# Kernel optimization log

Hardware: AMD Instinct MI355X
Metric: run time of the kernel (lower is better)

The kernel has to match this reference:

```python
import jax, jax.numpy as jnp
import numpy as np

K = 16  # centroids per codebook (4-bit LUT indices, blink-mm convention)


def _im2col(x, kh, kw, stride, pad):
    # x: [B, C, H, W] -> [B, P, C*kh*kw] with channel-major feature ordering
    # (each length-(kh*kw) subvector is one channel's patch, matching the
    #  per-channel codebook layout of the 3x3 AMM conv).
    B, C, H, W = x.shape
    xp = jnp.pad(x, ((0, 0), (0, 0), (pad, pad), (pad, pad)))
    Ho = (H + 2 * pad - kh) // stride + 1
    Wo = (W + 2 * pad - kw) // stride + 1
    cols = [xp[:, :, i:i + stride * Ho:stride, j:j + stride * Wo:stride]
            for i in range(kh) for j in range(kw)]  # fixed small loop (<=9)
    feat = jnp.stack(cols, axis=2)                      # [B, C, kh*kw, Ho, Wo]
    feat = feat.reshape(B, C * kh * kw, Ho, Wo)
    feat = feat.transpose(0, 2, 3, 1).reshape(B, Ho * Wo, C * kh * kw)
    return feat, Ho, Wo


def _amm_conv_bn_act(x, centroids, lut, scale, bias, kernel, stride, pad, relu):
    # Product-quantization approximate matmul conv:
    #  1) im2col, split feature dim D into ncodebooks subspaces of dim dsub
    #  2) nearest-centroid (L2) assignment per subspace -> 4-bit index
    #  3) gather+accumulate precomputed LUT dot products over codebooks
    #  4) folded BatchNorm affine + optional ReLU
    feat, Ho, Wo = _im2col(x, kernel, kernel, stride, pad)
    B, P, D = feat.shape
    ncb, k, dsub = centroids.shape
    xs = feat.reshape(B, P, ncb, dsub)
    dots = jnp.einsum('bpcd,ckd->bpck', xs, centroids)          # [B,P,ncb,K]
    c2 = jnp.sum(centroids * centroids, axis=-1)                # [ncb,K]
    idx = jnp.argmin(c2[None, None] - 2.0 * dots, axis=-1)      # [B,P,ncb]
    onehot = jax.nn.one_hot(idx, k, dtype=x.dtype)              # [B,P,ncb,K]
    out = jnp.einsum('bpck,cko->bpo', onehot, lut)              # LUT accumulate
    out = out * scale + bias                                    # folded BN
    if relu:
        out = jax.nn.relu(out)
    Cout = lut.shape[-1]
    return out.reshape(B, Ho, Wo, Cout).transpose(0, 3, 1, 2)


def setup_inputs() -> dict:
    key = jax.random.key(0)
    ks = jax.random.split(key, 16)
    inplanes, planes, width = 1024, 256, 256
    B, H, W = 32, 14, 14
    d = {}
    d['x'] = jax.random.normal(ks[0], (B, inplanes, H, W), dtype=jnp.float32)
    d['c1_centroids'] = jax.random.normal(ks[1], (inplanes // 4, K, 4), dtype=jnp.float32)
    d['c1_lut'] = jax.random.normal(ks[2], (inplanes // 4, K, width), dtype=jnp.float32) * 0.1
    d['c1_scale'] = jax.random.uniform(ks[3], (width,), dtype=jnp.float32, minval=0.5, maxval=1.5)
    d['c1_bias'] = jax.random.normal(ks[4], (width,), dtype=jnp.float32) * 0.1
    d['c2_centroids'] = jax.random.normal(ks[5], (width, K, 9), dtype=jnp.float32)
    d['c2_lut'] = jax.random.normal(ks[6], (width, K, width), dtype=jnp.float32) * 0.1
    d['c2_scale'] = jax.random.uniform(ks[7], (width,), dtype=jnp.float32, minval=0.5, maxval=1.5)
    d['c2_bias'] = jax.random.normal(ks[8], (width,), dtype=jnp.float32) * 0.1
    d['c3_centroids'] = jax.random.normal(ks[9], (width // 4, K, 4), dtype=jnp.float32)
    d['c3_lut'] = jax.random.normal(ks[10], (width // 4, K, planes * 4), dtype=jnp.float32) * 0.1
    d['c3_scale'] = jax.random.uniform(ks[11], (planes * 4,), dtype=jnp.float32, minval=0.5, maxval=1.5)
    d['c3_bias'] = jax.random.normal(ks[12], (planes * 4,), dtype=jnp.float32) * 0.1
    return d


def reference(x, c1_centroids, c1_lut, c1_scale, c1_bias,
              c2_centroids, c2_lut, c2_scale, c2_bias,
              c3_centroids, c3_lut, c3_scale, c3_bias):
    identity = x
    out = _amm_conv_bn_act(x, c1_centroids, c1_lut, c1_scale, c1_bias,
                           kernel=1, stride=1, pad=0, relu=True)
    out = _amm_conv_bn_act(out, c2_centroids, c2_lut, c2_scale, c2_bias,
                           kernel=3, stride=1, pad=1, relu=True)
    out = _amm_conv_bn_act(out, c3_centroids, c3_lut, c3_scale, c3_bias,
                           kernel=1, stride=1, pad=0, relu=False)
    # QuantizedAdd + QuantizedReLU (float reference math: add then relu)
    return jax.nn.relu(out + identity)
```

## Files before the change

kernel.cpp:

```cpp
#include <hip/hip_runtime.h>
#include <stdint.h>

#define PP 196
#define BP 6272


template <typename T>
__global__ __launch_bounds__(256) void assign_1x1(
    const T* __restrict__ in, const float* __restrict__ cents,
    uint32_t* __restrict__ idxp, int nchan) {
  __shared__ double s_cent[8][16][4];
  __shared__ double s_c2[8][16];
  const int chunk = blockIdx.y;
  const int t = threadIdx.x;
  for (int i = t; i < 8 * 16 * 4; i += 256)
    ((double*)s_cent)[i] = (double)cents[(size_t)chunk * 512 + i];
  __syncthreads();
  if (t < 128) {
    int cb_l = t >> 4, k = t & 15;
    double s = 0.0;
#pragma unroll
    for (int d = 0; d < 4; d++) { double c = s_cent[cb_l][k][d]; s += c * c; }
    s_c2[cb_l][k] = s;
  }
  __syncthreads();
  const int p = blockIdx.x * 256 + t;
  if (p >= BP) return;
  const unsigned b = (unsigned)p / 196u;
  const unsigned pr = (unsigned)p - b * 196u;
  const T* xb = in + ((size_t)b * nchan + chunk * 32) * PP + pr;
  double xv[32];
#pragma unroll
  for (int i = 0; i < 32; i++) xv[i] = (double)xb[(size_t)i * PP];
  uint32_t word = 0;
#pragma unroll
  for (int cb_l = 0; cb_l < 8; cb_l++) {
    double best = 1e300; int bi = 0;
#pragma unroll
    for (int k = 0; k < 16; k++) {
      double dot = 0.0;
#pragma unroll
      for (int d = 0; d < 4; d++) dot = fma(xv[cb_l * 4 + d], s_cent[cb_l][k][d], dot);
      double dist = s_c2[cb_l][k] - 2.0 * dot;
      if (dist < best) { best = dist; bi = k; }
    }
    word |= (uint32_t)bi << (4 * cb_l);
  }
  idxp[(size_t)chunk * BP + p] = word;
}

__global__ __launch_bounds__(256) void assign_3x3(
    const double* __restrict__ in, const float* __restrict__ cents,
    uint32_t* __restrict__ idxp) {
  __shared__ double s_cent[8][16][9];
  __shared__ double s_c2[8][16];
  const int chunk = blockIdx.y;
  const int c0 = chunk * 8;
  const int t = threadIdx.x;
  for (int i = t; i < 8 * 16 * 9; i += 256)
    ((double*)s_cent)[i] = (double)cents[(size_t)c0 * 144 + i];
  __syncthreads();
  if (t < 128) {
    int cb_l = t >> 4, k = t & 15;
    double s = 0.0;
#pragma unroll
    for (int d = 0; d < 9; d++) { double c = s_cent[cb_l][k][d]; s += c * c; }
    s_c2[cb_l][k] = s;
  }
  __syncthreads();
  const int p = blockIdx.x * 256 + t;
  if (p >= BP) return;
  const unsigned b = (unsigned)p / 196u;
  const unsigned pr = (unsigned)p - b * 196u;
  const int oh = pr / 14, ow = pr - oh * 14;
  uint32_t word = 0;
  for (int cb_l = 0; cb_l < 8; cb_l++) {
    const double* base = in + ((size_t)b * 256 + (c0 + cb_l)) * PP;
    double v[9];
#pragma unroll
    for (int i = 0; i < 3; i++) {
#pragma unroll
      for (int j = 0; j < 3; j++) {
        int hh = oh + i - 1, ww = ow + j - 1;
        bool ok = (hh >= 0) & (hh < 14) & (ww >= 0) & (ww < 14);
        v[i * 3 + j] = ok ? base[hh * 14 + ww] : 0.0;
      }
    }
    double best = 1e300; int bi = 0;
#pragma unroll
    for (int k = 0; k < 16; k++) {
      double dot = 0.0;
#pragma unroll
      for (int d = 0; d < 9; d++) dot = fma(v[d], s_cent[cb_l][k][d], dot);
      double dist = s_c2[cb_l][k] - 2.0 * dot;
      if (dist < best) { best = dist; bi = k; }
    }
    word |= (uint32_t)bi << (4 * cb_l);
  }
  idxp[(size_t)chunk * BP + p] = word;
}

template <int NCB, int NOUT, bool RELU, bool RES, typename OutT>
__global__ __launch_bounds__(512) void accum_kernel(
    const float* __restrict__ lut, const uint32_t* __restrict__ idxp,
    const float* __restrict__ scale, const float* __restrict__ bias,
    const float* __restrict__ res, OutT* __restrict__ out) {
  __shared__ float s_lut[16 * 16 * 36];
  const int t = threadIdx.x;
  const int lane = t & 63;
  const int wave = t >> 6;
  const int oquad = wave & 3;
  const int pg = wave >> 2;
  const int p = blockIdx.x * 128 + pg * 64 + lane;
  const int o_base = blockIdx.y * 16;
  const int r = t >> 1, h = t & 1;
  const int cb_ls = r >> 4, ks = r & 15;
  double a0 = 0.0, a1 = 0.0, a2 = 0.0, a3 = 0.0;
  constexpr int NCHUNK = NCB / 16;
  for (int ch = 0; ch < NCHUNK; ch++) {
    __syncthreads();
    uint32_t w0 = idxp[(size_t)(ch * 2) * BP + p];
    uint32_t w1 = idxp[(size_t)(ch * 2 + 1) * BP + p];
    {
      const float* g = lut + (((size_t)(ch * 16 + cb_ls)) * 16 + ks) * NOUT + o_base + h * 8;
      float4 va = *(const float4*)g;
      float4 vb = *(const float4*)(g + 4);
      float* sd = s_lut + cb_ls * 576 + ks * 36 + h * 8;
      *(float4*)sd = va;
      *(float4*)(sd + 4) = vb;
    }
    __syncthreads();
#pragma unroll
    for (int cb_l = 0; cb_l < 16; cb_l++) {
      uint32_t w = (cb_l < 8) ? w0 : w1;
      int idx = (int)((w >> (4 * (cb_l & 7))) & 15u);
      const float4 v = *(const float4*)(s_lut + cb_l * 576 + idx * 36 + oquad * 4);
      a0 += (double)v.x; a1 += (double)v.y; a2 += (double)v.z; a3 += (double)v.w;
    }
  }
  const unsigned b = (unsigned)p / 196u;
  const unsigned pr = (unsigned)p - b * 196u;
  const int o = o_base + oquad * 4;
  const float4 sc = *(const float4*)(scale + o);
  const float4 bs = *(const float4*)(bias + o);
  double r0 = a0 * (double)sc.x + (double)bs.x;
  double r1 = a1 * (double)sc.y + (double)bs.y;
  double r2 = a2 * (double)sc.z + (double)bs.z;
  double r3 = a3 * (double)sc.w + (double)bs.w;
  if (RES) {
    const float* rp = res + ((size_t)b * NOUT + o) * PP + pr;
    r0 += (double)rp[0 * PP]; r1 += (double)rp[1 * PP];
    r2 += (double)rp[2 * PP]; r3 += (double)rp[3 * PP];
  }
  if (RELU) {
    r0 = fmax(r0, 0.0); r1 = fmax(r1, 0.0);
    r2 = fmax(r2, 0.0); r3 = fmax(r3, 0.0);
  }
  OutT* op = out + ((size_t)b * NOUT + o) * PP + pr;
  op[0 * PP] = (OutT)r0; op[1 * PP] = (OutT)r1;
  op[2 * PP] = (OutT)r2; op[3 * PP] = (OutT)r3;
}


extern "C" void kernel_launch(void* const* d_in, const int* in_sizes, int n_in,
                              void* d_out, int out_size, void* d_ws, size_t ws_size,
                              hipStream_t stream) {
  const float* x   = (const float*)d_in[0];
  const float* c1c = (const float*)d_in[1];
  const float* c1l = (const float*)d_in[2];
  const float* c1s = (const float*)d_in[3];
  const float* c1b = (const float*)d_in[4];
  const float* c2c = (const float*)d_in[5];
  const float* c2l = (const float*)d_in[6];
  const float* c2s = (const float*)d_in[7];
  const float* c2b = (const float*)d_in[8];
  const float* c3c = (const float*)d_in[9];
  const float* c3l = (const float*)d_in[10];
  const float* c3s = (const float*)d_in[11];
  const float* c3b = (const float*)d_in[12];

  const size_t sz_i1 = (size_t)32 * BP * 4;
  const size_t sz_i2 = (size_t)32 * BP * 4;
  const size_t sz_i3 = (size_t)8 * BP * 4;
  const size_t sz_o64 = (size_t)BP * 256 * 8;

  char* w = (char*)d_ws;
  uint32_t* i1 = (uint32_t*)w; w += sz_i1;
  uint32_t* i2 = (uint32_t*)w; w += sz_i2;
  uint32_t* i3 = (uint32_t*)w; w += sz_i3;
  double *out1, *out2;
  if (ws_size >= sz_i1 + sz_i2 + sz_i3 + 2 * sz_o64) {
    out1 = (double*)w;
    out2 = (double*)(w + sz_o64);
  } else {
    out1 = (double*)d_out;
    out2 = out1 + (size_t)BP * 256;
  }

  const dim3 blkA(256), blkC(512);
  assign_1x1<float><<<dim3(25, 32), blkA, 0, stream>>>(x, c1c, i1, 1024);
  accum_kernel<256, 256, true, false, double><<<dim3(49, 16), blkC, 0, stream>>>(
      c1l, i1, c1s, c1b, nullptr, out1);
  assign_3x3<<<dim3(25, 32), blkA, 0, stream>>>(out1, c2c, i2);
  accum_kernel<256, 256, true, false, double><<<dim3(49, 16), blkC, 0, stream>>>(
      c2l, i2, c2s, c2b, nullptr, out2);
  assign_1x1<double><<<dim3(25, 8), blkA, 0, stream>>>(out2, c3c, i3, 256);
  accum_kernel<64, 1024, true, true, float><<<dim3(49, 64), blkC, 0, stream>>>(
      c3l, i3, c3s, c3b, x, (float*)d_out);
}
```

Baseline: 274.9 us.

## Double-buffer LUT loads via async LDS copies and use fp16 LUT for last conv

The accumulation kernel now prefetches the next chunk's LUT slice straight into shared memory with global_load_lds async copies. It double-buffers the slice with an XOR-swizzled layout and prefetches the index words, removing one barrier per chunk and the register round-trip. The final conv stage gets a new kernel that reads an fp16 copy of the LUT, converted on every call, and accumulates in fp32 instead of fp64. Assignment drops a multiply by folding the factor 0.5 into |c|^2. The fp16 LUT and fp32 accumulation lower precision and may change results against the float reference.

```diff
diff --git a/kernel.cpp b/kernel.cpp
--- a/kernel.cpp
+++ b/kernel.cpp
@@ -3,6 +3,19 @@
 
 #define PP 196
 #define BP 6272
+
+typedef _Float16 half_t;
+typedef half_t half8v __attribute__((ext_vector_type(8)));
+typedef half_t half4v __attribute__((ext_vector_type(4)));
+
+__device__ __forceinline__ void async_cp16(const void* g, void* l) {
+  __builtin_amdgcn_global_load_lds(
+      (const __attribute__((address_space(1))) void*)g,
+      (__attribute__((address_space(3))) void*)l, 16, 0, 0);
+}
+__device__ __forceinline__ void wait_vm0() {
+  __builtin_amdgcn_s_waitcnt(0x0f70);
+}
 
 
 template <typename T>
@@ -21,7 +34,7 @@
     double s = 0.0;
 #pragma unroll
     for (int d = 0; d < 4; d++) { double c = s_cent[cb_l][k][d]; s += c * c; }
-    s_c2[cb_l][k] = s;
+    s_c2[cb_l][k] = 0.5 * s;
   }
   __syncthreads();
   const int p = blockIdx.x * 256 + t;
@@ -41,7 +54,7 @@
       double dot = 0.0;
 #pragma unroll
       for (int d = 0; d < 4; d++) dot = fma(xv[cb_l * 4 + d], s_cent[cb_l][k][d], dot);
-      double dist = s_c2[cb_l][k] - 2.0 * dot;
+      double dist = s_c2[cb_l][k] - dot;
       if (dist < best) { best = dist; bi = k; }
     }
     word |= (uint32_t)bi << (4 * cb_l);
@@ -65,7 +78,7 @@
     double s = 0.0;
 #pragma unroll
     for (int d = 0; d < 9; d++) { double c = s_cent[cb_l][k][d]; s += c * c; }
-    s_c2[cb_l][k] = s;
+    s_c2[cb_l][k] = 0.5 * s;
   }
   __syncthreads();
   const int p = blockIdx.x * 256 + t;
@@ -92,7 +105,7 @@
       double dot = 0.0;
 #pragma unroll
       for (int d = 0; d < 9; d++) dot = fma(v[d], s_cent[cb_l][k][d], dot);
-      double dist = s_c2[cb_l][k] - 2.0 * dot;
+      double dist = s_c2[cb_l][k] - dot;
       if (dist < best) { best = dist; bi = k; }
     }
     word |= (uint32_t)bi << (4 * cb_l);
@@ -101,46 +114,57 @@
 }
 
 template <int NCB, int NOUT, bool RELU, bool RES, typename OutT>
-__global__ __launch_bounds__(512) void accum_kernel(
+__global__ __launch_bounds__(512) void accum_f64(
     const float* __restrict__ lut, const uint32_t* __restrict__ idxp,
     const float* __restrict__ scale, const float* __restrict__ bias,
     const float* __restrict__ res, OutT* __restrict__ out) {
-  __shared__ float s_lut[16 * 16 * 36];
+  __shared__ float s_lut[2][4096];
   const int t = threadIdx.x;
   const int lane = t & 63;
   const int wave = t >> 6;
-  const int oquad = wave & 3;
+  const int q = wave & 3;
   const int pg = wave >> 2;
   const int p = blockIdx.x * 128 + pg * 64 + lane;
   const int o_base = blockIdx.y * 16;
-  const int r = t >> 1, h = t & 1;
-  const int cb_ls = r >> 4, ks = r & 15;
-  double a0 = 0.0, a1 = 0.0, a2 = 0.0, a3 = 0.0;
+  const int sk = lane >> 2;
+  const int sq = (lane & 3) ^ ((sk >> 1) & 3);
+  const float* src0 = lut + ((size_t)(wave * 2) * 16 + sk) * NOUT + o_base + sq * 4;
+  const float* src1 = src0 + (size_t)16 * NOUT;
+  const size_t chunk_stride = (size_t)256 * NOUT;
   constexpr int NCHUNK = NCB / 16;
+
+  async_cp16(src0, &s_lut[0][wave * 2 * 256]);
+  async_cp16(src1, &s_lut[0][wave * 2 * 256 + 256]);
+  uint32_t w0 = idxp[p];
+  uint32_t w1 = idxp[(size_t)BP + p];
+  double a0 = 0, a1 = 0, a2 = 0, a3 = 0;
   for (int ch = 0; ch < NCHUNK; ch++) {
+    wait_vm0();
     __syncthreads();
-    uint32_t w0 = idxp[(size_t)(ch * 2) * BP + p];
-    uint32_t w1 = idxp[(size_t)(ch * 2 + 1) * BP + p];
-    {
-      const float* g = lut + (((size_t)(ch * 16 + cb_ls)) * 16 + ks) * NOUT + o_base + h * 8;
-      float4 va = *(const float4*)g;
-      float4 vb = *(const float4*)(g + 4);
-      float* sd = s_lut + cb_ls * 576 + ks * 36 + h * 8;
-      *(float4*)sd = va;
-      *(float4*)(sd + 4) = vb;
-    }
-    __syncthreads();
+    uint32_t nw0 = 0, nw1 = 0;
+    if (ch + 1 < NCHUNK) {
+      const float* s0 = src0 + (size_t)(ch + 1) * chunk_stride;
+      const float* s1 = src1 + (size_t)(ch + 1) * chunk_stride;
+      float* d0 = &s_lut[(ch + 1) & 1][wave * 2 * 256];
+      async_cp16(s0, d0);
+      async_cp16(s1, d0 + 256);
+      nw0 = idxp[(size_t)(2 * ch + 2) * BP + p];
+      nw1 = idxp[(size_t)(2 * ch + 3) * BP + p];
+    }
+    const char* base = (const char*)&s_lut[ch & 1][0];
 #pragma unroll
     for (int cb_l = 0; cb_l < 16; cb_l++) {
       uint32_t w = (cb_l < 8) ? w0 : w1;
-      int idx = (int)((w >> (4 * (cb_l & 7))) & 15u);
-      const float4 v = *(const float4*)(s_lut + cb_l * 576 + idx * 36 + oquad * 4);
+      uint32_t idx = (w >> (4 * (cb_l & 7))) & 15u;
+      uint32_t off = (idx << 6) + ((((uint32_t)q ^ (idx >> 1)) & 3u) << 4);
+      const float4 v = *(const float4*)(base + cb_l * 1024 + off);
       a0 += (double)v.x; a1 += (double)v.y; a2 += (double)v.z; a3 += (double)v.w;
     }
+    w0 = nw0; w1 = nw1;
   }
   const unsigned b = (unsigned)p / 196u;
   const unsigned pr = (unsigned)p - b * 196u;
-  const int o = o_base + oquad * 4;
+  const int o = o_base + q * 4;
   const float4 sc = *(const float4*)(scale + o);
   const float4 bs = *(const float4*)(bias + o);
   double r0 = a0 * (double)sc.x + (double)bs.x;
@@ -159,6 +183,85 @@
   OutT* op = out + ((size_t)b * NOUT + o) * PP + pr;
   op[0 * PP] = (OutT)r0; op[1 * PP] = (OutT)r1;
   op[2 * PP] = (OutT)r2; op[3 * PP] = (OutT)r3;
+}
+
+__global__ __launch_bounds__(256) void accum3_f16(
+    const half_t* __restrict__ lut16, const uint32_t* __restrict__ idxp,
+    const float* __restrict__ scale, const float* __restrict__ bias,
+    const float* __restrict__ res, float* __restrict__ out) {
+  __shared__ half_t s_lut[2][4096];
+  const int t = threadIdx.x;
+  const int lane = t & 63;
+  const int wave = t >> 6;
+  const int h = wave & 1;
+  const int pg = wave >> 1;
+  const int p = blockIdx.x * 128 + pg * 64 + lane;
+  const int o_base = blockIdx.y * 16;
+  const int s5 = lane & 31;
+  const int sk = s5 >> 1;
+  const int sh = (s5 & 1) ^ ((sk >> 2) & 1);
+  const int cbl0 = wave * 4 + (lane >> 5);
+  const half_t* src0 = lut16 + ((size_t)cbl0 * 16 + sk) * 1024 + o_base + sh * 8;
+  const half_t* src1 = src0 + (size_t)2 * 16 * 1024;
+  const size_t chunk_stride = (size_t)16 * 16 * 1024;
+  constexpr int NCHUNK = 4;
+
+  async_cp16(src0, &s_lut[0][wave * 2 * 512]);
+  async_cp16(src1, &s_lut[0][wave * 2 * 512 + 512]);
+  uint32_t w0 = idxp[p];
+  uint32_t w1 = idxp[(size_t)BP + p];
+  float a[8];
+#pragma unroll
+  for (int i = 0; i < 8; i++) a[i] = 0.f;
+  for (int ch = 0; ch < NCHUNK; ch++) {
+    wait_vm0();
+    __syncthreads();
+    uint32_t nw0 = 0, nw1 = 0;
+    if (ch + 1 < NCHUNK) {
+      const half_t* s0 = src0 + (size_t)(ch + 1) * chunk_stride;
+      const half_t* s1 = src1 + (size_t)(ch + 1) * chunk_stride;
+      half_t* d0 = &s_lut[(ch + 1) & 1][wave * 2 * 512];
+      async_cp16(s0, d0);
+      async_cp16(s1, d0 + 512);
+      nw0 = idxp[(size_t)(2 * ch + 2) * BP + p];
+      nw1 = idxp[(size_t)(2 * ch + 3) * BP + p];
+    }
+    const char* base = (const char*)&s_lut[ch & 1][0];
+#pragma unroll
+    for (int cb_l = 0; cb_l < 16; cb_l++) {
+      uint32_t w = (cb_l < 8) ? w0 : w1;
+      uint32_t idx = (w >> (4 * (cb_l & 7))) & 15u;
+      uint32_t off = (idx << 5) + ((((uint32_t)h ^ (idx >> 2)) & 1u) << 4);
+      const half8v v = *(const half8v*)(base + cb_l * 512 + off);
+#pragma unroll
+      for (int i = 0; i < 8; i++) a[i] += (float)v[i];
+    }
+    w0 = nw0; w1 = nw1;
+  }
+  const unsigned b = (unsigned)p / 196u;
+  const unsigned pr = (unsigned)p - b * 196u;
+  const int o = o_base + h * 8;
+  float r[8];
+#pragma unroll
+  for (int i = 0; i < 8; i++) r[i] = a[i] * scale[o + i] + bias[o + i];
+  const float* rp = res + ((size_t)b * 1024 + o) * PP + pr;
+  float* op = out + ((size_t)b * 1024 + o) * PP + pr;
+#pragma unroll
+  for (int i = 0; i < 8; i++) {
+    float v = fmaxf(r[i] + rp[(size_t)i * PP], 0.f);
+    op[(size_t)i * PP] = v;
+  }
+}
+
+__global__ __launch_bounds__(256) void cvt_f16(
+    const float* __restrict__ src, half_t* __restrict__ dst, int n) {
+  int i = (blockIdx.x * 256 + threadIdx.x) * 4;
+  if (i < n) {
+    float4 v = *(const float4*)(src + i);
+    half4v o;
+    o[0] = (half_t)v.x; o[1] = (half_t)v.y; o[2] = (half_t)v.z; o[3] = (half_t)v.w;
+    *(half4v*)(dst + i) = o;
+  }
 }
 
 
@@ -182,14 +285,19 @@
   const size_t sz_i1 = (size_t)32 * BP * 4;
   const size_t sz_i2 = (size_t)32 * BP * 4;
   const size_t sz_i3 = (size_t)8 * BP * 4;
+  const size_t sz_l16 = (size_t)64 * 16 * 1024 * 2;
   const size_t sz_o64 = (size_t)BP * 256 * 8;
 
   char* w = (char*)d_ws;
   uint32_t* i1 = (uint32_t*)w; w += sz_i1;
   uint32_t* i2 = (uint32_t*)w; w += sz_i2;
   uint32_t* i3 = (uint32_t*)w; w += sz_i3;
+  const size_t base_need = sz_i1 + sz_i2 + sz_i3;
+  bool use_f16 = (ws_size >= base_need + sz_l16);
+  half_t* l16 = (half_t*)w;
+  if (use_f16) w += sz_l16;
   double *out1, *out2;
-  if (ws_size >= sz_i1 + sz_i2 + sz_i3 + 2 * sz_o64) {
+  if (ws_size >= (size_t)(w - (char*)d_ws) + 2 * sz_o64) {
     out1 = (double*)w;
     out2 = (double*)(w + sz_o64);
   } else {
@@ -197,14 +305,20 @@
     out2 = out1 + (size_t)BP * 256;
   }
 
-  const dim3 blkA(256), blkC(512);
+  const dim3 blkA(256);
+  if (use_f16)
+    cvt_f16<<<dim3(1024), blkA, 0, stream>>>(c3l, l16, 64 * 16 * 1024);
   assign_1x1<float><<<dim3(25, 32), blkA, 0, stream>>>(x, c1c, i1, 1024);
-  accum_kernel<256, 256, true, false, double><<<dim3(49, 16), blkC, 0, stream>>>(
+  accum_f64<256, 256, true, false, double><<<dim3(49, 16), dim3(512), 0, stream>>>(
       c1l, i1, c1s, c1b, nullptr, out1);
   assign_3x3<<<dim3(25, 32), blkA, 0, stream>>>(out1, c2c, i2);
-  accum_kernel<256, 256, true, false, double><<<dim3(49, 16), blkC, 0, stream>>>(
+  accum_f64<256, 256, true, false, double><<<dim3(49, 16), dim3(512), 0, stream>>>(
       c2l, i2, c2s, c2b, nullptr, out2);
   assign_1x1<double><<<dim3(25, 8), blkA, 0, stream>>>(out2, c3c, i3, 256);
-  accum_kernel<64, 1024, true, true, float><<<dim3(49, 64), blkC, 0, stream>>>(
-      c3l, i3, c3s, c3b, x, (float*)d_out);
-}
+  if (use_f16)
+    accum3_f16<<<dim3(49, 64), blkA, 0, stream>>>(
+        l16, i3, c3s, c3b, x, (float*)d_out);
+  else
+    accum_f64<64, 1024, true, true, float><<<dim3(49, 64), dim3(512), 0, stream>>>(
+        c3l, i3, c3s, c3b, x, (float*)d_out);
+}
```

Result: slower. 307.8 us (+12.0%).
